# Kernel tuning notes

Measured on AMD Instinct MI355X. Metric: run time of the kernel, lower is better.

Reference implementation:

```python
import jax, jax.numpy as jnp
import numpy as np

D = 1024
N_HEADS = 16
HEAD_DIM = D // N_HEADS
EPS = 1e-09


def setup_inputs() -> dict:
    key = jax.random.key(0)
    ks = jax.random.split(key, 8)
    s = 0.02
    return {
        "x": jax.random.normal(ks[0], (2, 2048, D), jnp.float32),
        "Wq": jax.random.normal(ks[1], (D, D), jnp.float32) * s,
        "Wk": jax.random.normal(ks[2], (D, D), jnp.float32) * s,
        "Wv": jax.random.normal(ks[3], (D, D), jnp.float32) * s,
        "Wo": jax.random.normal(ks[4], (D, D), jnp.float32) * s,
        "W_up": jax.random.normal(ks[5], (4 * D, D), jnp.float32) * s,
        "W_down": jax.random.normal(ks[6], (D, 4 * D), jnp.float32) * s,
        "ln1_mean_scale": jnp.zeros((D,), jnp.float32),
        "ln1_std_scale": jnp.ones((D,), jnp.float32),
        "ln2_mean_scale": jnp.zeros((D,), jnp.float32),
        "ln2_std_scale": jnp.ones((D,), jnp.float32),
    }


def _ln(x, mean_scale, std_scale):
    mean = jnp.mean(x, axis=-1, keepdims=True)
    # torch .var() defaults to unbiased (ddof=1)
    std = jnp.sqrt(jnp.var(x, axis=-1, keepdims=True, ddof=1) + EPS)
    return (x - mean) / std * std_scale + mean_scale


def _attention(x, Wq, Wk, Wv, Wo):
    B, S, _ = x.shape
    # nn.Linear(bias=False): y = x @ W.T
    def heads(W):
        return (x @ W.T).reshape(B, S, N_HEADS, HEAD_DIM).transpose(0, 2, 1, 3)
    Q, K, V = heads(Wq), heads(Wk), heads(Wv)
    scale = jnp.sqrt(jnp.asarray(HEAD_DIM, Q.dtype))
    logits = jnp.einsum('bhqd,bhkd->bhqk', Q, K) / scale  # [B,H,S,S]
    causal = jnp.tril(jnp.ones((S, S), bool))
    logits = jnp.where(causal, logits, -jnp.inf)
    A = jax.nn.softmax(logits, axis=-1)
    preout = jnp.einsum('bhqk,bhkd->bhqd', A, V)  # [B,H,S,hd]
    # Wo.weight.T reshaped to (n_heads, d_head, d_model); per-head out then sum
    W_O = Wo.T.reshape(N_HEADS, HEAD_DIM, D)
    return jnp.einsum('bhsd,hdm->bsm', preout, W_O)


def _mlp(x, W_up, W_down):
    mid = jax.nn.gelu(x @ W_up.T, approximate=False)
    return mid @ W_down.T


def reference(x, Wq, Wk, Wv, Wo, W_up, W_down,
              ln1_mean_scale, ln1_std_scale, ln2_mean_scale, ln2_std_scale):
    x = x + _attention(_ln(x, ln1_mean_scale, ln1_std_scale), Wq, Wk, Wv, Wo)
    x = x + _mlp(_ln(x, ln2_mean_scale, ln2_std_scale), W_up, W_down)
    return x
```

## Files before the change

kernel.cpp:

```cpp
#include <hip/hip_runtime.h>
#include <hip/hip_bf16.h>
#include <cstdint>
#include <cstddef>

#define D_MODEL 1024
#define SEQ     2048
#define NTOK    4096
#define NH      16
#define HD      64

typedef __attribute__((ext_vector_type(8))) short sh8;
typedef __attribute__((ext_vector_type(4))) float f32x4;

#define GLL(g, s) __builtin_amdgcn_global_load_lds(                                   \
    (const __attribute__((address_space(1))) void*)(g),                               \
    (__attribute__((address_space(3))) void*)(s), 16, 0, 0)

__device__ __forceinline__ unsigned short f2b(float f) {
  union { float f; unsigned u; } v; v.f = f;
  unsigned r = v.u + 0x7FFFu + ((v.u >> 16) & 1u);
  return (unsigned short)(r >> 16);
}
__device__ __forceinline__ float b2f(unsigned short h) {
  union { unsigned u; float f; } v; v.u = ((unsigned)h) << 16;
  return v.f;
}

__global__ __launch_bounds__(256) void cast6_kernel(
    const float* __restrict__ q, const float* __restrict__ k, const float* __restrict__ v,
    const float* __restrict__ o, const float* __restrict__ u, const float* __restrict__ d,
    unsigned short* __restrict__ oq, unsigned short* __restrict__ ok,
    unsigned short* __restrict__ ov, unsigned short* __restrict__ oo,
    unsigned short* __restrict__ ou, unsigned short* __restrict__ od) {
  int bid = blockIdx.x;
  const float* src; unsigned short* dst; int base;
  if      (bid < 1024) { src = q; dst = oq; base = bid; }
  else if (bid < 2048) { src = k; dst = ok; base = bid - 1024; }
  else if (bid < 3072) { src = v; dst = ov; base = bid - 2048; }
  else if (bid < 4096) { src = o; dst = oo; base = bid - 3072; }
  else if (bid < 8192) { src = u; dst = ou; base = bid - 4096; }
  else                 { src = d; dst = od; base = bid - 8192; }
  int i = base * 1024 + threadIdx.x * 4;
  float4 vv = *(const float4*)(src + i);
  ushort4 w;
  w.x = f2b(vv.x); w.y = f2b(vv.y); w.z = f2b(vv.z); w.w = f2b(vv.w);
  *(ushort4*)(dst + i) = w;
}

__global__ __launch_bounds__(256) void ln_kernel(const float* __restrict__ x,
                                                 const float* __restrict__ msc,
                                                 const float* __restrict__ ssc,
                                                 unsigned short* __restrict__ out) {
  const int t = blockIdx.x;
  const int tid = threadIdx.x;
  const float4 v = ((const float4*)(x + (size_t)t * D_MODEL))[tid];
  float s = v.x + v.y + v.z + v.w;
  float q = v.x * v.x + v.y * v.y + v.z * v.z + v.w * v.w;
  #pragma unroll
  for (int off = 32; off; off >>= 1) {
    s += __shfl_xor(s, off);
    q += __shfl_xor(q, off);
  }
  __shared__ float sh[8];
  const int w = tid >> 6;
  if ((tid & 63) == 0) { sh[w * 2] = s; sh[w * 2 + 1] = q; }
  __syncthreads();
  s = sh[0] + sh[2] + sh[4] + sh[6];
  q = sh[1] + sh[3] + sh[5] + sh[7];
  const float mean = s * (1.0f / D_MODEL);
  const float var = (q - (float)D_MODEL * mean * mean) * (1.0f / (D_MODEL - 1));
  const float rstd = rsqrtf(var + 1e-9f);
  const float4 ms = ((const float4*)msc)[tid];
  const float4 ss = ((const float4*)ssc)[tid];
  ushort4 o;
  o.x = f2b((v.x - mean) * rstd * ss.x + ms.x);
  o.y = f2b((v.y - mean) * rstd * ss.y + ms.y);
  o.z = f2b((v.z - mean) * rstd * ss.z + ms.z);
  o.w = f2b((v.w - mean) * rstd * ss.w + ms.w);
  ((ushort4*)(out + (size_t)t * D_MODEL))[tid] = o;
}

__global__ __launch_bounds__(256) void reduce_ln_kernel(
    const unsigned short* __restrict__ p0, const unsigned short* __restrict__ p1,
    const float* __restrict__ x, const float* __restrict__ msc,
    const float* __restrict__ ssc, float* __restrict__ out,
    unsigned short* __restrict__ oln) {
  const int t = blockIdx.x;
  const int tid = threadIdx.x;
  const size_t base = (size_t)t * D_MODEL + tid * 4;
  ushort4 a = *(const ushort4*)(p0 + base);
  ushort4 b = *(const ushort4*)(p1 + base);
  float4 xv = *(const float4*)(x + base);
  float4 r;
  r.x = xv.x + b2f(a.x) + b2f(b.x);
  r.y = xv.y + b2f(a.y) + b2f(b.y);
  r.z = xv.z + b2f(a.z) + b2f(b.z);
  r.w = xv.w + b2f(a.w) + b2f(b.w);
  *(float4*)(out + base) = r;
  float s = r.x + r.y + r.z + r.w;
  float q = r.x * r.x + r.y * r.y + r.z * r.z + r.w * r.w;
  #pragma unroll
  for (int off = 32; off; off >>= 1) {
    s += __shfl_xor(s, off);
    q += __shfl_xor(q, off);
  }
  __shared__ float sh[8];
  const int w = tid >> 6;
  if ((tid & 63) == 0) { sh[w * 2] = s; sh[w * 2 + 1] = q; }
  __syncthreads();
  s = sh[0] + sh[2] + sh[4] + sh[6];
  q = sh[1] + sh[3] + sh[5] + sh[7];
  const float mean = s * (1.0f / D_MODEL);
  const float var = (q - (float)D_MODEL * mean * mean) * (1.0f / (D_MODEL - 1));
  const float rstd = rsqrtf(var + 1e-9f);
  const float4 ms = ((const float4*)msc)[tid];
  const float4 ss = ((const float4*)ssc)[tid];
  ushort4 o;
  o.x = f2b((r.x - mean) * rstd * ss.x + ms.x);
  o.y = f2b((r.y - mean) * rstd * ss.y + ms.y);
  o.z = f2b((r.z - mean) * rstd * ss.z + ms.z);
  o.w = f2b((r.w - mean) * rstd * ss.w + ms.w);
  *(ushort4*)(oln + base) = o;
}

__global__ __launch_bounds__(256) void reduce2_kernel(const unsigned short* __restrict__ p0,
                                                      const unsigned short* __restrict__ p1,
                                                      float* __restrict__ out) {
  int i = (blockIdx.x * 256 + threadIdx.x) * 4;
  ushort4 a = *(const ushort4*)(p0 + i);
  ushort4 b = *(const ushort4*)(p1 + i);
  float4 base = *(const float4*)(out + i);
  float4 r;
  r.x = base.x + b2f(a.x) + b2f(b.x);
  r.y = base.y + b2f(a.y) + b2f(b.y);
  r.z = base.z + b2f(a.z) + b2f(b.z);
  r.w = base.w + b2f(a.w) + b2f(b.w);
  *(float4*)(out + i) = r;
}

__global__ __launch_bounds__(256) void attn_combine_kernel(
    unsigned short* __restrict__ p0, const unsigned short* __restrict__ p1,
    const float* __restrict__ l0, const float* __restrict__ l1) {
  int i = (blockIdx.x * 256 + threadIdx.x) * 4;
  const int tok = i >> 10, ch = i & 1023;
  const int b = tok >> 11, s = tok & 2047, h = ch >> 6;
  const int lidx = ((b << 4) + h) * 2048 + s;
  const float inv = 1.0f / (l0[lidx] + l1[lidx]);
  ushort4 a = *(const ushort4*)(p0 + i);
  ushort4 c = *(const ushort4*)(p1 + i);
  ushort4 r;
  r.x = f2b((b2f(a.x) + b2f(c.x)) * inv);
  r.y = f2b((b2f(a.y) + b2f(c.y)) * inv);
  r.z = f2b((b2f(a.z) + b2f(c.z)) * inv);
  r.w = f2b((b2f(a.w) + b2f(c.w)) * inv);
  *(ushort4*)(p0 + i) = r;
}

__global__ __launch_bounds__(256) void vtrans_kernel(const unsigned short* __restrict__ qkv,
                                                     unsigned short* __restrict__ vt) {
  __shared__ unsigned short T[64][72];
  const int st = blockIdx.x;
  const int b  = blockIdx.y >> 4;
  const int dt = blockIdx.y & 15;
  const int tid = threadIdx.x;
  const int s0 = st * 64, d0 = dt * 64;
  const int r = tid >> 2, c0 = (tid & 3) * 16;
  const unsigned short* src = qkv + ((size_t)b * SEQ + s0 + r) * 3072 + 2 * D_MODEL + d0 + c0;
  *(uint4*)&T[r][c0]     = *(const uint4*)(src);
  *(uint4*)&T[r][c0 + 8] = *(const uint4*)(src + 8);
  __syncthreads();
  unsigned short buf[16] __attribute__((aligned(16)));
  #pragma unroll
  for (int j = 0; j < 16; j++) buf[j] = T[c0 + j][r];
  unsigned short* dst = vt + ((size_t)b * D_MODEL + d0 + r) * SEQ + s0 + c0;
  *(uint4*)(dst)     = *(uint4*)&buf[0];
  *(uint4*)(dst + 8) = *(uint4*)&buf[8];
}

template <int EP, int GX, int GY, int GZ, int CHX, int CHY>
__global__ __launch_bounds__(256) void gemm_nt(const unsigned short* __restrict__ A,
                                               const unsigned short* __restrict__ B,
                                               int N, int LD, int Kext,
                                               unsigned short* __restrict__ Cbf,
                                               unsigned short* __restrict__ Cbf2) {
  constexpr int NRX = GX / CHX;
  constexpr int NRY = GY / CHY;
  static_assert(NRX * NRY * GZ == 8, "rect count must equal 8 XCDs");
  __shared__ __align__(16) unsigned short As[128 * 64];
  __shared__ __align__(16) unsigned short Bs[128 * 64];
  const int tid = threadIdx.x;
  const int w = tid >> 6, l = tid & 63, ln = tid & 15, quad = (tid & 63) >> 4;
  const int wr = (w >> 1) * 64, wc = (w & 1) * 64;

  const int lb  = blockIdx.x;
  const int xcd = lb & 7, slot = lb >> 3;
  const int rx  = xcd % NRX, rem = xcd / NRX;
  const int ry  = rem % NRY, rz = rem / NRY;
  const int sx  = slot % CHX, sy = slot / CHX;
  const int bx  = rx * CHX + sx;
  const int by  = ry * CHY + sy;
  const int bz  = rz;

  const int m0 = by * 128, n0 = bx * 128;
  const int koff = bz * Kext;

  const int sr = l >> 3, sc = l & 7;
  const unsigned short* AgS = A + (size_t)(m0 + w * 32 + sr) * LD + koff + ((sc ^ sr) * 8);
  const unsigned short* BgS = B + (size_t)(n0 + w * 32 + sr) * LD + koff + ((sc ^ sr) * 8);
  unsigned short* AsW = &As[(w * 32) * 64];
  unsigned short* BsW = &Bs[(w * 32) * 64];

  f32x4 acc[4][4] = {};

  for (int k0 = 0; k0 < Kext; k0 += 64) {
    __syncthreads();
    #pragma unroll
    for (int off = 0; off < 32; off += 8) {
      GLL(AgS + k0 + (size_t)off * LD, AsW + off * 64);
      GLL(BgS + k0 + (size_t)off * LD, BsW + off * 64);
    }
    __syncthreads();
    sh8 af[2][4], bfr[2][4];
    #pragma unroll
    for (int kk = 0; kk < 2; kk++) {
      #pragma unroll
      for (int i = 0; i < 4; i++)
        af[kk][i]  = *(const sh8*)&As[(wr + i * 16 + ln) * 64 + (((kk * 4 + quad) ^ (ln & 7)) * 8)];
      #pragma unroll
      for (int j = 0; j < 4; j++)
        bfr[kk][j] = *(const sh8*)&Bs[(wc + j * 16 + ln) * 64 + (((kk * 4 + quad) ^ (ln & 7)) * 8)];
    }
    #pragma unroll
    for (int kk = 0; kk < 2; kk++)
      #pragma unroll
      for (int i = 0; i < 4; i++)
        #pragma unroll
        for (int j = 0; j < 4; j++)
          acc[i][j] = __builtin_amdgcn_mfma_f32_16x16x32_bf16(af[kk][i], bfr[kk][j], acc[i][j], 0, 0, 0);
  }

  unsigned short* C = bz ? Cbf2 : Cbf;
  #pragma unroll
  for (int i = 0; i < 4; i++) {
    #pragma unroll
    for (int rr = 0; rr < 4; rr++) {
      const int gm = m0 + wr + i * 16 + quad * 4 + rr;
      #pragma unroll
      for (int j = 0; j < 4; j++) {
        const int gn = n0 + wc + j * 16 + ln;
        float v = acc[i][j][rr];
        if (EP == 1) {
          const float vc = fminf(v, 8.0f);
          const float e = exp2f(2.3021906f * fmaf(0.044715f * vc * vc, vc, vc));
          v = v * e / (e + 1.0f);
        }
        C[(size_t)gm * N + gn] = f2b(v);
      }
    }
  }
}

__global__ __launch_bounds__(256) void attn_kernel(const unsigned short* __restrict__ qkv,
                                                   const unsigned short* __restrict__ vt,
                                                   unsigned short* __restrict__ p0,
                                                   unsigned short* __restrict__ p1,
                                                   float* __restrict__ l0,
                                                   float* __restrict__ l1) {
  const int bh = blockIdx.x;
  const int qt = (SEQ / 64 - 1) - blockIdx.y;
  const int z  = blockIdx.z;
  const int b = bh >> 4, h = bh & 15;
  const int tid = threadIdx.x;
  const int w = tid >> 6, l = tid & 63, ln = tid & 15, quad = (tid & 63) >> 4;
  const int q0 = qt * 64;

  __shared__ __align__(16) unsigned short Ks[64 * 64];
  __shared__ __align__(16) unsigned short Vs[64 * 64];
  __shared__ __align__(16) unsigned short Ps[4][16 * 72];

  const size_t rstride = 3 * D_MODEL;
  const unsigned short* Qg = qkv + (size_t)b * SEQ * rstride + h * HD;
  const unsigned short* Kg = Qg + D_MODEL;
  const unsigned short* Vg = vt + ((size_t)b * D_MODEL + h * HD) * SEQ;

  sh8 qf[2];
  {
    const unsigned short* qrow = Qg + (size_t)(q0 + w * 16 + ln) * rstride + quad * 8;
    qf[0] = *(const sh8*)(qrow);
    qf[1] = *(const sh8*)(qrow + 32);
  }

  const int lr3 = l >> 3, lp3 = l & 7;
  const int cS = (lp3 ^ lr3) * 8;
  const unsigned short* KgS = Kg + (size_t)(w * 16 + lr3) * rstride + cS;
  unsigned short* KsW = &Ks[(w * 16) * 64];
  const unsigned short* VgS = Vg + (size_t)(w * 16 + lr3) * SEQ + cS;
  unsigned short* VsW = &Vs[(w * 16) * 64];
  unsigned short* Psw = &Ps[w][0];

  f32x4 o[4] = {};
  float lpart[4] = {0.f, 0.f, 0.f, 0.f};
  const int rbase = q0 + w * 16 + quad * 4;

  auto tile = [&](int kt, bool diag) {
    __syncthreads();
    GLL(KgS + (size_t)(kt * 64) * rstride,     KsW);
    GLL(KgS + (size_t)(kt * 64 + 8) * rstride, KsW + 8 * 64);
    GLL(VgS + kt * 64,           VsW);
    GLL(VgS + 8 * SEQ + kt * 64, VsW + 8 * 64);
    __syncthreads();

    #pragma unroll
    for (int ct = 0; ct < 4; ct++) {
      const int k = ct * 16 + ln;
      f32x4 zz = {};
      zz = __builtin_amdgcn_mfma_f32_16x16x32_bf16(
          qf[0], *(const sh8*)&Ks[k * 64 + ((quad ^ (k & 7)) * 8)], zz, 0, 0, 0);
      zz = __builtin_amdgcn_mfma_f32_16x16x32_bf16(
          qf[1], *(const sh8*)&Ks[k * 64 + (((4 + quad) ^ (k & 7)) * 8)], zz, 0, 0, 0);
      const int cg = kt * 64 + ct * 16 + ln;
      #pragma unroll
      for (int rr = 0; rr < 4; rr++) {
        float e = exp2f(fmaf(zz[rr], 0.18033688011112042f, -5.770780163555853f));
        if (diag && cg > rbase + rr) e = 0.0f;
        lpart[rr] += e;
        Psw[(quad * 4 + rr) * 72 + ct * 16 + ln] = f2b(e);
      }
    }

    #pragma unroll
    for (int kk = 0; kk < 2; kk++) {
      sh8 pf = *(const sh8*)&Psw[ln * 72 + kk * 32 + quad * 8];
      #pragma unroll
      for (int c2 = 0; c2 < 4; c2++) {
        const int d = c2 * 16 + ln;
        sh8 vf = *(const sh8*)&Vs[d * 64 + ((((kk * 4 + quad) ^ (d & 7))) * 8)];
        o[c2] = __builtin_amdgcn_mfma_f32_16x16x32_bf16(pf, vf, o[c2], 0, 0, 0);
      }
    }
  };

  for (int kt = z; kt < qt; kt += 2) tile(kt, false);
  if ((qt & 1) == z) tile(qt, true);

  #pragma unroll
  for (int rr = 0; rr < 4; rr++) {
    #pragma unroll
    for (int off = 1; off < 16; off <<= 1) lpart[rr] += __shfl_xor(lpart[rr], off);
  }

  unsigned short* P = z ? p1 : p0;
  float* L = z ? l1 : l0;
  if (ln == 0) {
    #pragma unroll
    for (int rr = 0; rr < 4; rr++)
      L[((size_t)bh << 11) + q0 + w * 16 + quad * 4 + rr] = lpart[rr];
  }
  #pragma unroll
  for (int rr = 0; rr < 4; rr++) {
    const int row = q0 + w * 16 + quad * 4 + rr;
    const size_t base = ((size_t)b * SEQ + row) * D_MODEL + h * HD;
    #pragma unroll
    for (int c2 = 0; c2 < 4; c2++)
      P[base + c2 * 16 + ln] = f2b(o[c2][rr]);
  }
}

extern "C" void kernel_launch(void* const* d_in, const int* in_sizes, int n_in,
                              void* d_out, int out_size, void* d_ws, size_t ws_size,
                              hipStream_t stream) {
  const float* x    = (const float*)d_in[0];
  const float* Wq   = (const float*)d_in[1];
  const float* Wk   = (const float*)d_in[2];
  const float* Wv   = (const float*)d_in[3];
  const float* Wo   = (const float*)d_in[4];
  const float* Wup  = (const float*)d_in[5];
  const float* Wdn  = (const float*)d_in[6];
  const float* ln1m = (const float*)d_in[7];
  const float* ln1s = (const float*)d_in[8];
  const float* ln2m = (const float*)d_in[9];
  const float* ln2s = (const float*)d_in[10];
  float* out = (float*)d_out;

  unsigned short* ws = (unsigned short*)d_ws;
  size_t off = 0;
  unsigned short* wqkv = ws + off; off += (size_t)3072 * 1024;
  unsigned short* wo   = ws + off; off += (size_t)1024 * 1024;
  unsigned short* wup  = ws + off; off += (size_t)4096 * 1024;
  unsigned short* wdn  = ws + off; off += (size_t)1024 * 4096;
  unsigned short* xln  = ws + off; off += (size_t)NTOK * 1024;
  unsigned short* qkvb = ws + off; off += (size_t)NTOK * 3072;
  unsigned short* pre  = ws + off; off += (size_t)NTOK * 1024;
  unsigned short* mid  = qkvb;
  unsigned short* vtg  = xln;
  unsigned short* po0  = qkvb;
  unsigned short* po1  = qkvb + (size_t)NTOK * 1024;
  unsigned short* pd0  = ws;
  unsigned short* pd1  = xln;
  unsigned short* ap1  = (unsigned short*)out;
  float* al0 = (float*)wqkv;
  float* al1 = al0 + (size_t)2 * NH * SEQ;

  cast6_kernel<<<12288, 256, 0, stream>>>(Wq, Wk, Wv, Wo, Wup, Wdn,
      wqkv, wqkv + (size_t)1024 * 1024, wqkv + (size_t)2 * 1024 * 1024, wo, wup, wdn);

  ln_kernel<<<NTOK, 256, 0, stream>>>(x, ln1m, ln1s, xln);
  gemm_nt<0, 24, 32, 1, 12, 8><<<768, 256, 0, stream>>>(xln, wqkv, 3072, 1024, 1024, qkvb, nullptr);
  vtrans_kernel<<<dim3(32, 32), 256, 0, stream>>>(qkvb, vtg);
  attn_kernel<<<dim3(2 * NH, SEQ / 64, 2), 256, 0, stream>>>(qkvb, vtg, pre, ap1, al0, al1);
  attn_combine_kernel<<<4096, 256, 0, stream>>>(pre, ap1, al0, al1);
  gemm_nt<0, 8, 32, 2, 4, 16><<<512, 256, 0, stream>>>(pre, wo, 1024, 1024, 512, po0, po1);
  reduce_ln_kernel<<<NTOK, 256, 0, stream>>>(po0, po1, x, ln2m, ln2s, out, xln);
  gemm_nt<1, 32, 32, 1, 8, 16><<<1024, 256, 0, stream>>>(xln, wup, 4096, 1024, 1024, mid, nullptr);
  gemm_nt<0, 8, 32, 2, 8, 8><<<512, 256, 0, stream>>>(mid, wdn, 1024, 4096, 2048, pd0, pd1);
  reduce2_kernel<<<4096, 256, 0, stream>>>(pd0, pd1, out);
}
```

Measured before the change: 327.5 us.

## Drop attention split-K and combine kernel; fuse down-proj reduction via atomics

Attention now processes all key tiles in one block per query tile and normalizes by the row sum in-kernel, removing the two-way split, the partial-sum buffers and the combine kernel. The down-projection GEMM's split-K partials are accumulated directly into the fp32 output with atomic adds, replacing the bf16 partial stores and the separate reduce kernel. The attention grid halves, so blocks for late query tiles run longer with less parallelism. The atomics add contention and make the summation order nondeterministic.

```diff
diff --git a/kernel.cpp b/kernel.cpp
--- a/kernel.cpp
+++ b/kernel.cpp
@@ -123,39 +123,6 @@
   *(ushort4*)(oln + base) = o;
 }
 
-__global__ __launch_bounds__(256) void reduce2_kernel(const unsigned short* __restrict__ p0,
-                                                      const unsigned short* __restrict__ p1,
-                                                      float* __restrict__ out) {
-  int i = (blockIdx.x * 256 + threadIdx.x) * 4;
-  ushort4 a = *(const ushort4*)(p0 + i);
-  ushort4 b = *(const ushort4*)(p1 + i);
-  float4 base = *(const float4*)(out + i);
-  float4 r;
-  r.x = base.x + b2f(a.x) + b2f(b.x);
-  r.y = base.y + b2f(a.y) + b2f(b.y);
-  r.z = base.z + b2f(a.z) + b2f(b.z);
-  r.w = base.w + b2f(a.w) + b2f(b.w);
-  *(float4*)(out + i) = r;
-}
-
-__global__ __launch_bounds__(256) void attn_combine_kernel(
-    unsigned short* __restrict__ p0, const unsigned short* __restrict__ p1,
-    const float* __restrict__ l0, const float* __restrict__ l1) {
-  int i = (blockIdx.x * 256 + threadIdx.x) * 4;
-  const int tok = i >> 10, ch = i & 1023;
-  const int b = tok >> 11, s = tok & 2047, h = ch >> 6;
-  const int lidx = ((b << 4) + h) * 2048 + s;
-  const float inv = 1.0f / (l0[lidx] + l1[lidx]);
-  ushort4 a = *(const ushort4*)(p0 + i);
-  ushort4 c = *(const ushort4*)(p1 + i);
-  ushort4 r;
-  r.x = f2b((b2f(a.x) + b2f(c.x)) * inv);
-  r.y = f2b((b2f(a.y) + b2f(c.y)) * inv);
-  r.z = f2b((b2f(a.z) + b2f(c.z)) * inv);
-  r.w = f2b((b2f(a.w) + b2f(c.w)) * inv);
-  *(ushort4*)(p0 + i) = r;
-}
-
 __global__ __launch_bounds__(256) void vtrans_kernel(const unsigned short* __restrict__ qkv,
                                                      unsigned short* __restrict__ vt) {
   __shared__ unsigned short T[64][72];
@@ -239,7 +206,7 @@
           acc[i][j] = __builtin_amdgcn_mfma_f32_16x16x32_bf16(af[kk][i], bfr[kk][j], acc[i][j], 0, 0, 0);
   }
 
-  unsigned short* C = bz ? Cbf2 : Cbf;
+  unsigned short* C = (EP == 2) ? Cbf : (bz ? Cbf2 : Cbf);
   #pragma unroll
   for (int i = 0; i < 4; i++) {
     #pragma unroll
@@ -249,12 +216,16 @@
       for (int j = 0; j < 4; j++) {
         const int gn = n0 + wc + j * 16 + ln;
         float v = acc[i][j][rr];
-        if (EP == 1) {
-          const float vc = fminf(v, 8.0f);
-          const float e = exp2f(2.3021906f * fmaf(0.044715f * vc * vc, vc, vc));
-          v = v * e / (e + 1.0f);
+        if (EP == 2) {
+          unsafeAtomicAdd((float*)C + (size_t)gm * N + gn, v);
+        } else {
+          if (EP == 1) {
+            const float vc = fminf(v, 8.0f);
+            const float e = exp2f(2.3021906f * fmaf(0.044715f * vc * vc, vc, vc));
+            v = v * e / (e + 1.0f);
+          }
+          C[(size_t)gm * N + gn] = f2b(v);
         }
-        C[(size_t)gm * N + gn] = f2b(v);
       }
     }
   }
@@ -262,13 +233,9 @@
 
 __global__ __launch_bounds__(256) void attn_kernel(const unsigned short* __restrict__ qkv,
                                                    const unsigned short* __restrict__ vt,
-                                                   unsigned short* __restrict__ p0,
-                                                   unsigned short* __restrict__ p1,
-                                                   float* __restrict__ l0,
-                                                   float* __restrict__ l1) {
+                                                   unsigned short* __restrict__ pre) {
   const int bh = blockIdx.x;
   const int qt = (SEQ / 64 - 1) - blockIdx.y;
-  const int z  = blockIdx.z;
   const int b = bh >> 4, h = bh & 15;
   const int tid = threadIdx.x;
   const int w = tid >> 6, l = tid & 63, ln = tid & 15, quad = (tid & 63) >> 4;
@@ -340,8 +307,8 @@
     }
   };
 
-  for (int kt = z; kt < qt; kt += 2) tile(kt, false);
-  if ((qt & 1) == z) tile(qt, true);
+  for (int kt = 0; kt < qt; kt++) tile(kt, false);
+  tile(qt, true);
 
   #pragma unroll
   for (int rr = 0; rr < 4; rr++) {
@@ -349,20 +316,14 @@
     for (int off = 1; off < 16; off <<= 1) lpart[rr] += __shfl_xor(lpart[rr], off);
   }
 
-  unsigned short* P = z ? p1 : p0;
-  float* L = z ? l1 : l0;
-  if (ln == 0) {
-    #pragma unroll
-    for (int rr = 0; rr < 4; rr++)
-      L[((size_t)bh << 11) + q0 + w * 16 + quad * 4 + rr] = lpart[rr];
-  }
   #pragma unroll
   for (int rr = 0; rr < 4; rr++) {
+    const float inv = 1.0f / lpart[rr];
     const int row = q0 + w * 16 + quad * 4 + rr;
     const size_t base = ((size_t)b * SEQ + row) * D_MODEL + h * HD;
     #pragma unroll
     for (int c2 = 0; c2 < 4; c2++)
-      P[base + c2 * 16 + ln] = f2b(o[c2][rr]);
+      pre[base + c2 * 16 + ln] = f2b(o[c2][rr] * inv);
   }
 }
 
@@ -395,11 +356,6 @@
   unsigned short* vtg  = xln;
   unsigned short* po0  = qkvb;
   unsigned short* po1  = qkvb + (size_t)NTOK * 1024;
-  unsigned short* pd0  = ws;
-  unsigned short* pd1  = xln;
-  unsigned short* ap1  = (unsigned short*)out;
-  float* al0 = (float*)wqkv;
-  float* al1 = al0 + (size_t)2 * NH * SEQ;
 
   cast6_kernel<<<12288, 256, 0, stream>>>(Wq, Wk, Wv, Wo, Wup, Wdn,
       wqkv, wqkv + (size_t)1024 * 1024, wqkv + (size_t)2 * 1024 * 1024, wo, wup, wdn);
@@ -407,11 +363,10 @@
   ln_kernel<<<NTOK, 256, 0, stream>>>(x, ln1m, ln1s, xln);
   gemm_nt<0, 24, 32, 1, 12, 8><<<768, 256, 0, stream>>>(xln, wqkv, 3072, 1024, 1024, qkvb, nullptr);
   vtrans_kernel<<<dim3(32, 32), 256, 0, stream>>>(qkvb, vtg);
-  attn_kernel<<<dim3(2 * NH, SEQ / 64, 2), 256, 0, stream>>>(qkvb, vtg, pre, ap1, al0, al1);
-  attn_combine_kernel<<<4096, 256, 0, stream>>>(pre, ap1, al0, al1);
+  attn_kernel<<<dim3(2 * NH, SEQ / 64), 256, 0, stream>>>(qkvb, vtg, pre);
   gemm_nt<0, 8, 32, 2, 4, 16><<<512, 256, 0, stream>>>(pre, wo, 1024, 1024, 512, po0, po1);
   reduce_ln_kernel<<<NTOK, 256, 0, stream>>>(po0, po1, x, ln2m, ln2s, out, xln);
   gemm_nt<1, 32, 32, 1, 8, 16><<<1024, 256, 0, stream>>>(xln, wup, 4096, 1024, 1024, mid, nullptr);
-  gemm_nt<0, 8, 32, 2, 8, 8><<<512, 256, 0, stream>>>(mid, wdn, 1024, 4096, 2048, pd0, pd1);
-  reduce2_kernel<<<4096, 256, 0, stream>>>(pd0, pd1, out);
-}
+  gemm_nt<2, 8, 32, 2, 8, 8><<<512, 256, 0, stream>>>(mid, wdn, 1024, 4096, 2048,
+                                                      (unsigned short*)out, nullptr);
+}
```

Measured after the change: 356.0 us. +8.7%, slower.

## Fuse split-K down-proj reduction via fp32 atomics and merge cast with LN

Applied to the files above, without the earlier changes.

Replaces the down-projection split-K GEMM that wrote two bf16 partial buffers plus a separate reduce kernel with a dedicated GEMM that atomically adds fp32 partials directly into the residual output. Also merges the weight-cast and first layernorm kernels into one launch. This removes a kernel launch and a full read/write pass of partials, at the cost of global atomic traffic and nondeterministic summation order.

```diff
diff --git a/kernel.cpp b/kernel.cpp
--- a/kernel.cpp
+++ b/kernel.cpp
@@ -26,58 +26,57 @@
   return v.f;
 }
 
-__global__ __launch_bounds__(256) void cast6_kernel(
+__global__ __launch_bounds__(256) void castln_kernel(
     const float* __restrict__ q, const float* __restrict__ k, const float* __restrict__ v,
     const float* __restrict__ o, const float* __restrict__ u, const float* __restrict__ d,
     unsigned short* __restrict__ oq, unsigned short* __restrict__ ok,
     unsigned short* __restrict__ ov, unsigned short* __restrict__ oo,
-    unsigned short* __restrict__ ou, unsigned short* __restrict__ od) {
-  int bid = blockIdx.x;
-  const float* src; unsigned short* dst; int base;
-  if      (bid < 1024) { src = q; dst = oq; base = bid; }
-  else if (bid < 2048) { src = k; dst = ok; base = bid - 1024; }
-  else if (bid < 3072) { src = v; dst = ov; base = bid - 2048; }
-  else if (bid < 4096) { src = o; dst = oo; base = bid - 3072; }
-  else if (bid < 8192) { src = u; dst = ou; base = bid - 4096; }
-  else                 { src = d; dst = od; base = bid - 8192; }
-  int i = base * 1024 + threadIdx.x * 4;
-  float4 vv = *(const float4*)(src + i);
-  ushort4 w;
-  w.x = f2b(vv.x); w.y = f2b(vv.y); w.z = f2b(vv.z); w.w = f2b(vv.w);
-  *(ushort4*)(dst + i) = w;
-}
-
-__global__ __launch_bounds__(256) void ln_kernel(const float* __restrict__ x,
-                                                 const float* __restrict__ msc,
-                                                 const float* __restrict__ ssc,
-                                                 unsigned short* __restrict__ out) {
-  const int t = blockIdx.x;
-  const int tid = threadIdx.x;
-  const float4 v = ((const float4*)(x + (size_t)t * D_MODEL))[tid];
-  float s = v.x + v.y + v.z + v.w;
-  float q = v.x * v.x + v.y * v.y + v.z * v.z + v.w * v.w;
+    unsigned short* __restrict__ ou, unsigned short* __restrict__ od,
+    const float* __restrict__ x, const float* __restrict__ msc,
+    const float* __restrict__ ssc, unsigned short* __restrict__ xout) {
+  const int bid = blockIdx.x;
+  const int tid = threadIdx.x;
+  __shared__ float sh[8];
+  if (bid < 12288) {
+    const float* src; unsigned short* dst; int base;
+    if      (bid < 1024) { src = q; dst = oq; base = bid; }
+    else if (bid < 2048) { src = k; dst = ok; base = bid - 1024; }
+    else if (bid < 3072) { src = v; dst = ov; base = bid - 2048; }
+    else if (bid < 4096) { src = o; dst = oo; base = bid - 3072; }
+    else if (bid < 8192) { src = u; dst = ou; base = bid - 4096; }
+    else                 { src = d; dst = od; base = bid - 8192; }
+    int i = base * 1024 + tid * 4;
+    float4 vv = *(const float4*)(src + i);
+    ushort4 w;
+    w.x = f2b(vv.x); w.y = f2b(vv.y); w.z = f2b(vv.z); w.w = f2b(vv.w);
+    *(ushort4*)(dst + i) = w;
+    return;
+  }
+  const int t = bid - 12288;
+  const float4 vv = ((const float4*)(x + (size_t)t * D_MODEL))[tid];
+  float s = vv.x + vv.y + vv.z + vv.w;
+  float qs = vv.x * vv.x + vv.y * vv.y + vv.z * vv.z + vv.w * vv.w;
   #pragma unroll
   for (int off = 32; off; off >>= 1) {
     s += __shfl_xor(s, off);
-    q += __shfl_xor(q, off);
-  }
-  __shared__ float sh[8];
+    qs += __shfl_xor(qs, off);
+  }
   const int w = tid >> 6;
-  if ((tid & 63) == 0) { sh[w * 2] = s; sh[w * 2 + 1] = q; }
+  if ((tid & 63) == 0) { sh[w * 2] = s; sh[w * 2 + 1] = qs; }
   __syncthreads();
   s = sh[0] + sh[2] + sh[4] + sh[6];
-  q = sh[1] + sh[3] + sh[5] + sh[7];
+  qs = sh[1] + sh[3] + sh[5] + sh[7];
   const float mean = s * (1.0f / D_MODEL);
-  const float var = (q - (float)D_MODEL * mean * mean) * (1.0f / (D_MODEL - 1));
+  const float var = (qs - (float)D_MODEL * mean * mean) * (1.0f / (D_MODEL - 1));
   const float rstd = rsqrtf(var + 1e-9f);
   const float4 ms = ((const float4*)msc)[tid];
   const float4 ss = ((const float4*)ssc)[tid];
-  ushort4 o;
-  o.x = f2b((v.x - mean) * rstd * ss.x + ms.x);
-  o.y = f2b((v.y - mean) * rstd * ss.y + ms.y);
-  o.z = f2b((v.z - mean) * rstd * ss.z + ms.z);
-  o.w = f2b((v.w - mean) * rstd * ss.w + ms.w);
-  ((ushort4*)(out + (size_t)t * D_MODEL))[tid] = o;
+  ushort4 oo4;
+  oo4.x = f2b((vv.x - mean) * rstd * ss.x + ms.x);
+  oo4.y = f2b((vv.y - mean) * rstd * ss.y + ms.y);
+  oo4.z = f2b((vv.z - mean) * rstd * ss.z + ms.z);
+  oo4.w = f2b((vv.w - mean) * rstd * ss.w + ms.w);
+  ((ushort4*)(xout + (size_t)t * D_MODEL))[tid] = oo4;
 }
 
 __global__ __launch_bounds__(256) void reduce_ln_kernel(
@@ -123,21 +122,6 @@
   *(ushort4*)(oln + base) = o;
 }
 
-__global__ __launch_bounds__(256) void reduce2_kernel(const unsigned short* __restrict__ p0,
-                                                      const unsigned short* __restrict__ p1,
-                                                      float* __restrict__ out) {
-  int i = (blockIdx.x * 256 + threadIdx.x) * 4;
-  ushort4 a = *(const ushort4*)(p0 + i);
-  ushort4 b = *(const ushort4*)(p1 + i);
-  float4 base = *(const float4*)(out + i);
-  float4 r;
-  r.x = base.x + b2f(a.x) + b2f(b.x);
-  r.y = base.y + b2f(a.y) + b2f(b.y);
-  r.z = base.z + b2f(a.z) + b2f(b.z);
-  r.w = base.w + b2f(a.w) + b2f(b.w);
-  *(float4*)(out + i) = r;
-}
-
 __global__ __launch_bounds__(256) void attn_combine_kernel(
     unsigned short* __restrict__ p0, const unsigned short* __restrict__ p1,
     const float* __restrict__ l0, const float* __restrict__ l1) {
@@ -260,6 +244,78 @@
   }
 }
 
+__global__ __launch_bounds__(256) void gemm_dn(const unsigned short* __restrict__ A,
+                                               const unsigned short* __restrict__ B,
+                                               float* __restrict__ out) {
+  constexpr int N = 1024, LD = 4096, Kext = 2048;
+  constexpr int NRX = 1, NRY = 4, CHX = 8, CHY = 8;
+  __shared__ __align__(16) unsigned short As[128 * 64];
+  __shared__ __align__(16) unsigned short Bs[128 * 64];
+  const int tid = threadIdx.x;
+  const int w = tid >> 6, l = tid & 63, ln = tid & 15, quad = (tid & 63) >> 4;
+  const int wr = (w >> 1) * 64, wc = (w & 1) * 64;
+
+  const int lb  = blockIdx.x;
+  const int xcd = lb & 7, slot = lb >> 3;
+  const int rx  = xcd % NRX, rem = xcd / NRX;
+  const int ry  = rem % NRY, rz = rem / NRY;
+  const int sx  = slot % CHX, sy = slot / CHX;
+  const int bx  = rx * CHX + sx;
+  const int by  = ry * CHY + sy;
+  const int bz  = rz;
+
+  const int m0 = by * 128, n0 = bx * 128;
+  const int koff = bz * Kext;
+
+  const int sr = l >> 3, sc = l & 7;
+  const unsigned short* AgS = A + (size_t)(m0 + w * 32 + sr) * LD + koff + ((sc ^ sr) * 8);
+  const unsigned short* BgS = B + (size_t)(n0 + w * 32 + sr) * LD + koff + ((sc ^ sr) * 8);
+  unsigned short* AsW = &As[(w * 32) * 64];
+  unsigned short* BsW = &Bs[(w * 32) * 64];
+
+  f32x4 acc[4][4] = {};
+
+  for (int k0 = 0; k0 < Kext; k0 += 64) {
+    __syncthreads();
+    #pragma unroll
+    for (int off = 0; off < 32; off += 8) {
+      GLL(AgS + k0 + (size_t)off * LD, AsW + off * 64);
+      GLL(BgS + k0 + (size_t)off * LD, BsW + off * 64);
+    }
+    __syncthreads();
+    sh8 af[2][4], bfr[2][4];
+    #pragma unroll
+    for (int kk = 0; kk < 2; kk++) {
+      #pragma unroll
+      for (int i = 0; i < 4; i++)
+        af[kk][i]  = *(const sh8*)&As[(wr + i * 16 + ln) * 64 + (((kk * 4 + quad) ^ (ln & 7)) * 8)];
+      #pragma unroll
+      for (int j = 0; j < 4; j++)
+        bfr[kk][j] = *(const sh8*)&Bs[(wc + j * 16 + ln) * 64 + (((kk * 4 + quad) ^ (ln & 7)) * 8)];
+    }
+    #pragma unroll
+    for (int kk = 0; kk < 2; kk++)
+      #pragma unroll
+      for (int i = 0; i < 4; i++)
+        #pragma unroll
+        for (int j = 0; j < 4; j++)
+          acc[i][j] = __builtin_amdgcn_mfma_f32_16x16x32_bf16(af[kk][i], bfr[kk][j], acc[i][j], 0, 0, 0);
+  }
+
+  #pragma unroll
+  for (int i = 0; i < 4; i++) {
+    #pragma unroll
+    for (int rr = 0; rr < 4; rr++) {
+      const int gm = m0 + wr + i * 16 + quad * 4 + rr;
+      #pragma unroll
+      for (int j = 0; j < 4; j++) {
+        const int gn = n0 + wc + j * 16 + ln;
+        unsafeAtomicAdd(out + (size_t)gm * N + gn, acc[i][j][rr]);
+      }
+    }
+  }
+}
+
 __global__ __launch_bounds__(256) void attn_kernel(const unsigned short* __restrict__ qkv,
                                                    const unsigned short* __restrict__ vt,
                                                    unsigned short* __restrict__ p0,
@@ -395,16 +451,14 @@
   unsigned short* vtg  = xln;
   unsigned short* po0  = qkvb;
   unsigned short* po1  = qkvb + (size_t)NTOK * 1024;
-  unsigned short* pd0  = ws;
-  unsigned short* pd1  = xln;
   unsigned short* ap1  = (unsigned short*)out;
   float* al0 = (float*)wqkv;
   float* al1 = al0 + (size_t)2 * NH * SEQ;
 
-  cast6_kernel<<<12288, 256, 0, stream>>>(Wq, Wk, Wv, Wo, Wup, Wdn,
-      wqkv, wqkv + (size_t)1024 * 1024, wqkv + (size_t)2 * 1024 * 1024, wo, wup, wdn);
-
-  ln_kernel<<<NTOK, 256, 0, stream>>>(x, ln1m, ln1s, xln);
+  castln_kernel<<<16384, 256, 0, stream>>>(Wq, Wk, Wv, Wo, Wup, Wdn,
+      wqkv, wqkv + (size_t)1024 * 1024, wqkv + (size_t)2 * 1024 * 1024, wo, wup, wdn,
+      x, ln1m, ln1s, xln);
+
   gemm_nt<0, 24, 32, 1, 12, 8><<<768, 256, 0, stream>>>(xln, wqkv, 3072, 1024, 1024, qkvb, nullptr);
   vtrans_kernel<<<dim3(32, 32), 256, 0, stream>>>(qkvb, vtg);
   attn_kernel<<<dim3(2 * NH, SEQ / 64, 2), 256, 0, stream>>>(qkvb, vtg, pre, ap1, al0, al1);
@@ -412,6 +466,5 @@
   gemm_nt<0, 8, 32, 2, 4, 16><<<512, 256, 0, stream>>>(pre, wo, 1024, 1024, 512, po0, po1);
   reduce_ln_kernel<<<NTOK, 256, 0, stream>>>(po0, po1, x, ln2m, ln2s, out, xln);
   gemm_nt<1, 32, 32, 1, 8, 16><<<1024, 256, 0, stream>>>(xln, wup, 4096, 1024, 1024, mid, nullptr);
-  gemm_nt<0, 8, 32, 2, 8, 8><<<512, 256, 0, stream>>>(mid, wdn, 1024, 4096, 2048, pd0, pd1);
-  reduce2_kernel<<<4096, 256, 0, stream>>>(pd0, pd1, out);
-}
+  gemm_dn<<<512, 256, 0, stream>>>(mid, wdn, out);
+}
```

After: 350.5 us. 1.07x slower.

## Switch GEMM to 32x32x16 MFMA with padded row-group LDS layout

Applied to the files above, without the earlier changes.

Replaces the 16x16x32 bf16 MFMA tiling (4x4 accumulators per wave) with 32x32x16 MFMA (2x2 f32x16 accumulators), so each wave issues fewer, larger matrix instructions and reuses each loaded fragment across more output. LDS is reorganised into 16 groups of 8 rows, each padded to 520 elements, to avoid bank conflicts under the new fragment access pattern. The epilogue index mapping is rewritten to match the 32x32 accumulator layout. This adds register pressure from the larger accumulators and depends on the padding scheme staying compatible with global_load_lds writes.

```diff
diff --git a/kernel.cpp b/kernel.cpp
--- a/kernel.cpp
+++ b/kernel.cpp
@@ -11,6 +11,7 @@
 
 typedef __attribute__((ext_vector_type(8))) short sh8;
 typedef __attribute__((ext_vector_type(4))) float f32x4;
+typedef __attribute__((ext_vector_type(16))) float f32x16;
 
 #define GLL(g, s) __builtin_amdgcn_global_load_lds(                                   \
     (const __attribute__((address_space(1))) void*)(g),                               \
@@ -186,11 +187,13 @@
   constexpr int NRX = GX / CHX;
   constexpr int NRY = GY / CHY;
   static_assert(NRX * NRY * GZ == 8, "rect count must equal 8 XCDs");
-  __shared__ __align__(16) unsigned short As[128 * 64];
-  __shared__ __align__(16) unsigned short Bs[128 * 64];
+  constexpr int GRP = 520;
+  __shared__ __align__(16) unsigned short As[16 * GRP];
+  __shared__ __align__(16) unsigned short Bs[16 * GRP];
   const int tid = threadIdx.x;
-  const int w = tid >> 6, l = tid & 63, ln = tid & 15, quad = (tid & 63) >> 4;
-  const int wr = (w >> 1) * 64, wc = (w & 1) * 64;
+  const int w = tid >> 6, l = tid & 63;
+  const int lm = l & 31, lh = l >> 5;
+  const int wrow = (w >> 1) * 64, wcol = (w & 1) * 64;
 
   const int lb  = blockIdx.x;
   const int xcd = lb & 7, slot = lb >> 3;
@@ -207,48 +210,55 @@
   const int sr = l >> 3, sc = l & 7;
   const unsigned short* AgS = A + (size_t)(m0 + w * 32 + sr) * LD + koff + ((sc ^ sr) * 8);
   const unsigned short* BgS = B + (size_t)(n0 + w * 32 + sr) * LD + koff + ((sc ^ sr) * 8);
-  unsigned short* AsW = &As[(w * 32) * 64];
-  unsigned short* BsW = &Bs[(w * 32) * 64];
-
-  f32x4 acc[4][4] = {};
+  unsigned short* AsW = &As[(w * 4) * GRP];
+  unsigned short* BsW = &Bs[(w * 4) * GRP];
+
+  f32x16 acc[2][2] = {};
 
   for (int k0 = 0; k0 < Kext; k0 += 64) {
     __syncthreads();
     #pragma unroll
     for (int off = 0; off < 32; off += 8) {
-      GLL(AgS + k0 + (size_t)off * LD, AsW + off * 64);
-      GLL(BgS + k0 + (size_t)off * LD, BsW + off * 64);
+      GLL(AgS + k0 + (size_t)off * LD, AsW + (off >> 3) * GRP);
+      GLL(BgS + k0 + (size_t)off * LD, BsW + (off >> 3) * GRP);
     }
     __syncthreads();
-    sh8 af[2][4], bfr[2][4];
-    #pragma unroll
-    for (int kk = 0; kk < 2; kk++) {
-      #pragma unroll
-      for (int i = 0; i < 4; i++)
-        af[kk][i]  = *(const sh8*)&As[(wr + i * 16 + ln) * 64 + (((kk * 4 + quad) ^ (ln & 7)) * 8)];
-      #pragma unroll
-      for (int j = 0; j < 4; j++)
-        bfr[kk][j] = *(const sh8*)&Bs[(wc + j * 16 + ln) * 64 + (((kk * 4 + quad) ^ (ln & 7)) * 8)];
-    }
-    #pragma unroll
-    for (int kk = 0; kk < 2; kk++)
-      #pragma unroll
-      for (int i = 0; i < 4; i++)
+    sh8 af[2][4], bf2[2][4];
+    #pragma unroll
+    for (int i = 0; i < 2; i++) {
+      const int r = wrow + i * 32 + lm;
+      const int gb = (r >> 3) * GRP + (r & 7) * 64;
+      #pragma unroll
+      for (int s = 0; s < 4; s++)
+        af[i][s] = *(const sh8*)&As[gb + (((2 * s + lh) ^ (r & 7)) * 8)];
+    }
+    #pragma unroll
+    for (int j = 0; j < 2; j++) {
+      const int r = wcol + j * 32 + lm;
+      const int gb = (r >> 3) * GRP + (r & 7) * 64;
+      #pragma unroll
+      for (int s = 0; s < 4; s++)
+        bf2[j][s] = *(const sh8*)&Bs[gb + (((2 * s + lh) ^ (r & 7)) * 8)];
+    }
+    #pragma unroll
+    for (int s = 0; s < 4; s++)
+      #pragma unroll
+      for (int i = 0; i < 2; i++)
         #pragma unroll
-        for (int j = 0; j < 4; j++)
-          acc[i][j] = __builtin_amdgcn_mfma_f32_16x16x32_bf16(af[kk][i], bfr[kk][j], acc[i][j], 0, 0, 0);
+        for (int j = 0; j < 2; j++)
+          acc[i][j] = __builtin_amdgcn_mfma_f32_32x32x16_bf16(af[i][s], bf2[j][s], acc[i][j], 0, 0, 0);
   }
 
   unsigned short* C = bz ? Cbf2 : Cbf;
   #pragma unroll
-  for (int i = 0; i < 4; i++) {
-    #pragma unroll
-    for (int rr = 0; rr < 4; rr++) {
-      const int gm = m0 + wr + i * 16 + quad * 4 + rr;
-      #pragma unroll
-      for (int j = 0; j < 4; j++) {
-        const int gn = n0 + wc + j * 16 + ln;
-        float v = acc[i][j][rr];
+  for (int i = 0; i < 2; i++) {
+    #pragma unroll
+    for (int j = 0; j < 2; j++) {
+      #pragma unroll
+      for (int reg = 0; reg < 16; reg++) {
+        const int gm = m0 + wrow + i * 32 + (reg & 3) + 8 * (reg >> 2) + 4 * lh;
+        const int gn = n0 + wcol + j * 32 + lm;
+        float v = acc[i][j][reg];
         if (EP == 1) {
           const float vc = fminf(v, 8.0f);
           const float e = exp2f(2.3021906f * fmaf(0.044715f * vc * vc, vc, vc));
```

Result: no change. 330.9 us (+1.0%).
